# Performance work log

Measured on AMD Instinct MI355X. Metric: run time of the kernel, lower is better.

Reference implementation:

```python
import jax, jax.numpy as jnp
import numpy as np

N_NODES = 50000


def _gcn(x, row, col, w, b, n):
    # add self loops
    loops = jnp.arange(n, dtype=row.dtype)
    row = jnp.concatenate([row, loops])
    col = jnp.concatenate([col, loops])
    h = x @ w  # [N, out]
    deg = jax.ops.segment_sum(jnp.ones(col.shape, h.dtype), col, num_segments=n)
    dinv = jnp.where(deg > 0, deg ** -0.5, 0.0)
    norm = dinv[row] * dinv[col]  # [E+N]
    msg = norm[:, None] * h[row]
    out = jax.ops.segment_sum(msg, col, num_segments=n)
    return out + b


def _edgeconv(x, row, col, w1, b1, w2, b2, n):
    x_i = x[col]            # target features
    x_j = x[row]            # source features
    t = jnp.concatenate([x_i, x_j - x_i], axis=1)  # [E, 2*hidden]
    m = jax.nn.relu(t @ w1 + b1) @ w2 + b2          # [E, hidden]
    agg = jax.ops.segment_max(m, col, num_segments=n)
    # PyG fills empty segments with 0, segment_max fills with -inf
    return jnp.where(jnp.isfinite(agg), agg, 0.0)


def setup_inputs() -> dict:
    key = jax.random.key(0)
    ks = jax.random.split(key, 10)
    n, e = N_NODES, 800000
    cin, ch, cout = 32, 64, 16
    x = jax.random.normal(ks[0], (n, cin), dtype=jnp.float32)
    edge_index = jax.random.randint(ks[1], (2, e), 0, n, dtype=jnp.int64)

    def glorot(k, shape):
        lim = (6.0 / (shape[0] + shape[1])) ** 0.5
        return jax.random.uniform(k, shape, jnp.float32, -lim, lim)

    return {
        "x": x,
        "edge_index": edge_index,
        "gcn1_w": glorot(ks[2], (cin, ch)),
        "gcn1_b": jnp.zeros((ch,), jnp.float32),
        "edge_w1": glorot(ks[3], (2 * ch, ch)),
        "edge_b1": jnp.zeros((ch,), jnp.float32),
        "edge_w2": glorot(ks[4], (ch, ch)),
        "edge_b2": jnp.zeros((ch,), jnp.float32),
        "gcn2_w": glorot(ks[5], (ch, cout)),
        "gcn2_b": jnp.zeros((cout,), jnp.float32),
    }


def reference(x, edge_index, gcn1_w, gcn1_b, edge_w1, edge_b1, edge_w2, edge_b2, gcn2_w, gcn2_b):
    n = x.shape[0]
    row, col = edge_index[0], edge_index[1]
    h = jnp.tanh(_gcn(x, row, col, gcn1_w, gcn1_b, n))
    h = jax.nn.relu(_edgeconv(h, row, col, edge_w1, edge_b1, edge_w2, edge_b2, n))
    out = _gcn(h, row, col, gcn2_w, gcn2_b, n)
    return out
```

## Files before the change

### kernel.cpp

```cpp
#include <hip/hip_runtime.h>


typedef __attribute__((ext_vector_type(8))) short short8;
typedef __attribute__((ext_vector_type(4))) float f32x4;
typedef __attribute__((ext_vector_type(8))) _Float16 f16x8;
typedef __attribute__((ext_vector_type(4))) _Float16 f16x4;
typedef __attribute__((ext_vector_type(2))) _Float16 f16x2;

#define FILL_CH 4096

__device__ __forceinline__ unsigned short f2bf(float x) {
    unsigned int u = __float_as_uint(x);
    return (unsigned short)((u + 0x7FFFu + ((u >> 16) & 1u)) >> 16);
}
__device__ __forceinline__ float bf2f(unsigned short h) {
    return __uint_as_float(((unsigned int)h) << 16);
}
__device__ __forceinline__ void splitT(float u, short& hi, short& lo) {
    unsigned int ub = __float_as_uint(u);
    hi = (short)(ub >> 16);
    float r = u - __uint_as_float(ub & 0xFFFF0000u);
    lo = (short)(__float_as_uint(r) >> 16);
}
__device__ __forceinline__ f16x8 relu8(f16x8 v) {
    f16x8 z = {0, 0, 0, 0, 0, 0, 0, 0};
#if __has_builtin(__builtin_elementwise_max)
    return __builtin_elementwise_max(v, z);
#else
    f16x8 o;
#pragma unroll
    for (int j = 0; j < 8; ++j) o[j] = v[j] > (_Float16)0 ? v[j] : (_Float16)0;
    return o;
#endif
}

#define ROR_ADD(s, CTRL)                                                         \
    s += __int_as_float(__builtin_amdgcn_update_dpp(                             \
        0, __float_as_int(s), (CTRL), 0xf, 0xf, false))
#define ROR8_ADD(s) ROR_ADD(s, 0x128)

__global__ __launch_bounds__(256) void k_cast_count(
        const int* __restrict__ col, const float4* __restrict__ x4,
        f16x4* __restrict__ xh4, int* __restrict__ bcnt, int E, int m4, int nb) {
    __shared__ int cnt[512];
    int tid = threadIdx.x;
    for (int i = tid; i < nb; i += 256) cnt[i] = 0;
    __syncthreads();
    int e0 = blockIdx.x * FILL_CH;
#pragma unroll
    for (int i = 0; i < 16; ++i) {
        int e = e0 + tid + i * 256;
        if (e < E) atomicAdd(&cnt[col[e] >> 7], 1);
    }
    int nth = gridDim.x * 256;
    for (int idx = blockIdx.x * 256 + tid; idx < m4; idx += nth) {
        float4 v = x4[idx];
        f16x4 o;
        o[0] = (_Float16)v.x; o[1] = (_Float16)v.y;
        o[2] = (_Float16)v.z; o[3] = (_Float16)v.w;
        xh4[idx] = o;
    }
    __syncthreads();
    for (int i = tid; i < nb; i += 256)
        if (cnt[i]) atomicAdd(&bcnt[i], cnt[i]);
}

__global__ __launch_bounds__(512) void k_bucket_scan(
        const int* __restrict__ bcnt, int* __restrict__ bbase,
        int* __restrict__ bcur, int* __restrict__ ptr, int nb, int n, int E) {
    __shared__ int wt[8];
    int tid = threadIdx.x;
    int lane = tid & 63, w = tid >> 6;
    int v = (tid < nb) ? bcnt[tid] : 0;
    int s = v;
    for (int off = 1; off < 64; off <<= 1) {
        int t = __shfl_up(s, off, 64);
        if (lane >= off) s += t;
    }
    if (lane == 63) wt[w] = s;
    __syncthreads();
    int pre = 0;
    for (int i = 0; i < 8; ++i) if (i < w) pre += wt[i];
    int excl = pre + s - v;
    if (tid < nb) { bbase[tid] = excl; bcur[tid] = excl; }
    if (tid == nb) bbase[tid] = E;
    if (tid == 0) ptr[n] = E;
}

__global__ __launch_bounds__(256) void k_fill_a(const int* __restrict__ row,
                                                const int* __restrict__ col,
                                                int* __restrict__ bcur,
                                                int2* __restrict__ stage, int E, int nb) {
    __shared__ int cnt[512];
    __shared__ int base[512];
    int tid = threadIdx.x;
    int e0 = blockIdx.x * FILL_CH;
    for (int i = tid; i < nb; i += 256) cnt[i] = 0;
    __syncthreads();
    int r[16], c[16];
#pragma unroll
    for (int i = 0; i < 16; ++i) {
        int e = e0 + tid + i * 256;
        if (e < E) {
            r[i] = row[e]; c[i] = col[e];
            atomicAdd(&cnt[c[i] >> 7], 1);
        } else c[i] = -1;
    }
    __syncthreads();
    for (int i = tid; i < nb; i += 256)
        base[i] = cnt[i] ? atomicAdd(&bcur[i], cnt[i]) : 0;
    __syncthreads();
    for (int i = tid; i < nb; i += 256) cnt[i] = 0;
    __syncthreads();
#pragma unroll
    for (int i = 0; i < 16; ++i) {
        if (c[i] >= 0) {
            int b = c[i] >> 7;
            int lp = atomicAdd(&cnt[b], 1);
            stage[base[b] + lp] = make_int2(r[i], c[i]);
        }
    }
}

__global__ __launch_bounds__(256) void k_fill_b2(
        const int* __restrict__ bbase, const int* __restrict__ bcur_end,
        const int2* __restrict__ stage, int* __restrict__ ptr,
        float* __restrict__ dinv, int* __restrict__ csr, int n) {
    __shared__ int lcnt[128];
    __shared__ int lcur[128];
    __shared__ int wtotS;
    int b = blockIdx.x, tid = threadIdx.x;
    int c0 = b << 7;
    int start = bbase[b], end = bcur_end[b];
    if (tid < 128) lcnt[tid] = 0;
    __syncthreads();
    for (int p = start + tid; p < end; p += 256)
        atomicAdd(&lcnt[stage[p].y & 127], 1);
    __syncthreads();
    int lane = tid & 63, w = tid >> 6;
    int v = (tid < 128) ? lcnt[tid] : 0;
    int s = v;
    for (int off = 1; off < 64; off <<= 1) {
        int t = __shfl_up(s, off, 64);
        if (lane >= off) s += t;
    }
    if (tid == 63) wtotS = s;
    __syncthreads();
    int excl = s - v + ((w == 1) ? wtotS : 0);
    if (tid < 128) {
        int c = c0 + tid;
        int basep = start + excl;
        lcur[tid] = basep;
        if (c < n) {
            ptr[c] = basep;
            dinv[c] = rsqrtf((float)(v + 1));
        }
    }
    __syncthreads();
    for (int p = start + tid; p < end; p += 256) {
        int2 rc = stage[p];
        int pos = atomicAdd(&lcur[rc.y & 127], 1);
        csr[pos] = rc.x;
    }
}

__global__ __launch_bounds__(256) void k_gather32(
        const int* __restrict__ ptr, const int* __restrict__ csr_row,
        const float* __restrict__ x, const _Float16* __restrict__ xh,
        const float* __restrict__ dinv, float* __restrict__ agg, int n) {
    int wid = blockIdx.x * 4 + (threadIdx.x >> 6);
    if (wid >= n) return;
    int lane = threadIdx.x & 63;
    int f4 = lane & 7, slot = lane >> 3;
    int v = wid;
    int start = ptr[v], end = ptr[v + 1];
    const f16x4* xh4 = (const f16x4*)xh;
    float sx = 0.f, sy = 0.f, sz = 0.f, sw = 0.f;
    int p = start + slot;
    int r = (p < end) ? csr_row[p] : 0;
    while (p < end) {
        int rcur = r;
        int pn = p + 8;
        if (pn < end) r = csr_row[pn];
        float dr = dinv[rcur];
        f16x4 xv = xh4[(size_t)rcur * 8 + f4];
        sx = fmaf(dr, (float)xv[0], sx);
        sy = fmaf(dr, (float)xv[1], sy);
        sz = fmaf(dr, (float)xv[2], sz);
        sw = fmaf(dr, (float)xv[3], sw);
        p = pn;
    }
    ROR8_ADD(sx); ROR8_ADD(sy); ROR8_ADD(sz); ROR8_ADD(sw);
#pragma unroll
    for (int off = 16; off < 64; off <<= 1) {
        sx += __shfl_xor(sx, off); sy += __shfl_xor(sy, off);
        sz += __shfl_xor(sz, off); sw += __shfl_xor(sw, off);
    }
    if (slot == 0) {
        float dv = dinv[v], d2 = dv * dv;
        float4 xv = ((const float4*)x)[(size_t)v * 8 + f4];
        float4 o;
        o.x = dv * sx + d2 * xv.x;
        o.y = dv * sy + d2 * xv.y;
        o.z = dv * sz + d2 * xv.z;
        o.w = dv * sw + d2 * xv.w;
        ((float4*)agg)[(size_t)v * 8 + f4] = o;
    }
}

__global__ __launch_bounds__(256, 1) void k_h1tab(
        const float* __restrict__ agg, const float* __restrict__ gw,
        const float* __restrict__ gb, const float* __restrict__ w1,
        const float* __restrict__ b1,
        _Float16* __restrict__ atab, _Float16* __restrict__ btab, int ntiles) {
    __shared__ float tileS[4][16 * 66];
    int lane = threadIdx.x & 63;
    int wv = threadIdx.x >> 6;
    int n16 = lane & 15, q = lane >> 4;
    float* T = tileS[wv];

    short8 gh[4], gl[4];
    float gbias[4];
#pragma unroll
    for (int t = 0; t < 4; ++t) {
        gbias[t] = gb[t * 16 + n16];
        short8 hh, ll;
#pragma unroll
        for (int j = 0; j < 8; ++j) {
            float w = gw[(q * 8 + j) * 64 + t * 16 + n16];
            unsigned short wh = f2bf(w);
            hh[j] = (short)wh;
            ll[j] = (short)f2bf(w - bf2f(wh));
        }
        gh[t] = hh; gl[t] = ll;
    }
    short8 th[4][2], tl[4][2], uh[4][2], ul[4][2];
    float bias1[4];
#pragma unroll
    for (int t = 0; t < 4; ++t) {
        bias1[t] = b1[t * 16 + n16];
#pragma unroll
        for (int ck = 0; ck < 2; ++ck) {
            short8 h1v, l1v, h2v, l2v;
#pragma unroll
            for (int j = 0; j < 8; ++j) {
                int d = ck * 32 + q * 8 + j;
                float wbv = w1[(64 + d) * 64 + t * 16 + n16];
                float wtv = w1[d * 64 + t * 16 + n16] - wbv;
                unsigned short x1 = f2bf(wtv);
                h1v[j] = (short)x1; l1v[j] = (short)f2bf(wtv - bf2f(x1));
                unsigned short x2 = f2bf(wbv);
                h2v[j] = (short)x2; l2v[j] = (short)f2bf(wbv - bf2f(x2));
            }
            th[t][ck] = h1v; tl[t][ck] = l1v;
            uh[t][ck] = h2v; ul[t][ck] = l2v;
        }
    }

    int nwaves = gridDim.x * 4;
    int wid = blockIdx.x * 4 + wv;
    for (int tile = wid; tile < ntiles; tile += nwaves) {
        int v0 = tile * 16;
        const float4* a4 = (const float4*)(agg + (size_t)(v0 + n16) * 32);
        float4 A0 = a4[2 * q], A1 = a4[2 * q + 1];
        float a[8] = {A0.x, A0.y, A0.z, A0.w, A1.x, A1.y, A1.z, A1.w};
        short8 ah, al;
#pragma unroll
        for (int j = 0; j < 8; ++j) { short h, l; splitT(a[j], h, l); ah[j] = h; al[j] = l; }
#pragma unroll
        for (int t = 0; t < 4; ++t) {
            f32x4 acc = (f32x4){gbias[t], gbias[t], gbias[t], gbias[t]};
            acc = __builtin_amdgcn_mfma_f32_16x16x32_bf16(ah, gh[t], acc, 0, 0, 0);
            acc = __builtin_amdgcn_mfma_f32_16x16x32_bf16(al, gh[t], acc, 0, 0, 0);
            acc = __builtin_amdgcn_mfma_f32_16x16x32_bf16(ah, gl[t], acc, 0, 0, 0);
#pragma unroll
            for (int i = 0; i < 4; ++i)
                T[(q * 4 + i) * 66 + t * 16 + n16] = tanhf(acc[i]);
        }
        float b[16];
#pragma unroll
        for (int j = 0; j < 8; ++j) {
            b[j]     = T[n16 * 66 + q * 8 + j];
            b[8 + j] = T[n16 * 66 + 32 + q * 8 + j];
        }
        short8 ah0, ah1, al0, al1;
#pragma unroll
        for (int j = 0; j < 8; ++j) {
            short h, l;
            splitT(b[j], h, l);      ah0[j] = h; al0[j] = l;
            splitT(b[8 + j], h, l);  ah1[j] = h; al1[j] = l;
        }
#pragma unroll
        for (int t = 0; t < 4; ++t) {
            f32x4 aa = (f32x4){bias1[t], bias1[t], bias1[t], bias1[t]};
            aa = __builtin_amdgcn_mfma_f32_16x16x32_bf16(ah0, th[t][0], aa, 0, 0, 0);
            aa = __builtin_amdgcn_mfma_f32_16x16x32_bf16(ah1, th[t][1], aa, 0, 0, 0);
            aa = __builtin_amdgcn_mfma_f32_16x16x32_bf16(al0, th[t][0], aa, 0, 0, 0);
            aa = __builtin_amdgcn_mfma_f32_16x16x32_bf16(al1, th[t][1], aa, 0, 0, 0);
            aa = __builtin_amdgcn_mfma_f32_16x16x32_bf16(ah0, tl[t][0], aa, 0, 0, 0);
            aa = __builtin_amdgcn_mfma_f32_16x16x32_bf16(ah1, tl[t][1], aa, 0, 0, 0);
            f32x4 bb = (f32x4){0.f, 0.f, 0.f, 0.f};
            bb = __builtin_amdgcn_mfma_f32_16x16x32_bf16(ah0, uh[t][0], bb, 0, 0, 0);
            bb = __builtin_amdgcn_mfma_f32_16x16x32_bf16(ah1, uh[t][1], bb, 0, 0, 0);
            bb = __builtin_amdgcn_mfma_f32_16x16x32_bf16(al0, uh[t][0], bb, 0, 0, 0);
            bb = __builtin_amdgcn_mfma_f32_16x16x32_bf16(al1, uh[t][1], bb, 0, 0, 0);
            bb = __builtin_amdgcn_mfma_f32_16x16x32_bf16(ah0, ul[t][0], bb, 0, 0, 0);
            bb = __builtin_amdgcn_mfma_f32_16x16x32_bf16(ah1, ul[t][1], bb, 0, 0, 0);
#pragma unroll
            for (int i = 0; i < 4; ++i) {
                size_t off = (size_t)(v0 + q * 4 + i) * 64 + t * 16 + n16;
                atab[off] = (_Float16)aa[i];
                btab[off] = (_Float16)bb[i];
            }
        }
    }
}

__global__ __launch_bounds__(256) void k_edge_mlp(
        const int* __restrict__ ptr, const int* __restrict__ csr_row,
        const _Float16* __restrict__ atab, const _Float16* __restrict__ btab,
        const float* __restrict__ w2, const float* __restrict__ b2,
        const float* __restrict__ wg, _Float16* __restrict__ h2h, int n) {
    int lane = threadIdx.x & 63;
    int n16 = lane & 15, q = lane >> 4;

    f16x8 wh[4][2];
    float bias[4];
    float wgf[4][4];
#pragma unroll
    for (int t = 0; t < 4; ++t) {
        bias[t] = b2[t * 16 + n16];
#pragma unroll
        for (int jj = 0; jj < 4; ++jj)
            wgf[t][jj] = wg[(t * 16 + n16) * 16 + q * 4 + jj];
#pragma unroll
        for (int ck = 0; ck < 2; ++ck) {
            f16x8 hh;
#pragma unroll
            for (int j = 0; j < 8; ++j)
                hh[j] = (_Float16)w2[(ck * 32 + q * 8 + j) * 64 + t * 16 + n16];
            wh[t][ck] = hh;
        }
    }

    int nwaves = gridDim.x * 4;
    int wid = blockIdx.x * 4 + (threadIdx.x >> 6);

    for (int c = wid; c < n; c += nwaves) {
        int st = ptr[c], ed = ptr[c + 1];
        const f16x8* a8 = (const f16x8*)(atab + (size_t)c * 64);
        f16x8 A0 = a8[q], A1 = a8[4 + q];
        float red[4] = {0.f, 0.f, 0.f, 0.f};

        int p0 = st;
        int nfull = (ed - st) >> 4;
        for (int ft = 0; ft < nfull; ++ft, p0 += 16) {
            int r = csr_row[p0 + n16];
            const f16x8* b8 = (const f16x8*)(btab + (size_t)r * 64);
            f16x8 u0 = relu8(A0 + b8[q]);
            f16x8 u1 = relu8(A1 + b8[4 + q]);
#pragma unroll
            for (int t = 0; t < 4; ++t) {
                f32x4 acc = (f32x4){bias[t], bias[t], bias[t], bias[t]};
                acc = __builtin_amdgcn_mfma_f32_16x16x32_f16(u0, wh[t][0], acc, 0, 0, 0);
                acc = __builtin_amdgcn_mfma_f32_16x16x32_f16(u1, wh[t][1], acc, 0, 0, 0);
                red[t] = fmaxf(red[t], fmaxf(fmaxf(acc[0], acc[1]), fmaxf(acc[2], acc[3])));
            }
        }
        int rem = ed - p0;
        if (rem > 0) {
            f16x8 u0 = {0, 0, 0, 0, 0, 0, 0, 0};
            f16x8 u1 = {0, 0, 0, 0, 0, 0, 0, 0};
            if (n16 < rem) {
                int r = csr_row[p0 + n16];
                const f16x8* b8 = (const f16x8*)(btab + (size_t)r * 64);
                u0 = relu8(A0 + b8[q]);
                u1 = relu8(A1 + b8[4 + q]);
            }
#pragma unroll
            for (int t = 0; t < 4; ++t) {
                f32x4 acc = (f32x4){bias[t], bias[t], bias[t], bias[t]};
                acc = __builtin_amdgcn_mfma_f32_16x16x32_f16(u0, wh[t][0], acc, 0, 0, 0);
                acc = __builtin_amdgcn_mfma_f32_16x16x32_f16(u1, wh[t][1], acc, 0, 0, 0);
#pragma unroll
                for (int i = 0; i < 4; ++i)
                    if (q * 4 + i < rem) red[t] = fmaxf(red[t], acc[i]);
            }
        }
#pragma unroll
        for (int t = 0; t < 4; ++t) {
            red[t] = fmaxf(red[t], __shfl_xor(red[t], 16));
            red[t] = fmaxf(red[t], __shfl_xor(red[t], 32));
        }
        float part[4];
#pragma unroll
        for (int jj = 0; jj < 4; ++jj) {
            part[jj] = red[0] * wgf[0][jj];
            part[jj] = fmaf(red[1], wgf[1][jj], part[jj]);
            part[jj] = fmaf(red[2], wgf[2][jj], part[jj]);
            part[jj] = fmaf(red[3], wgf[3][jj], part[jj]);
            ROR_ADD(part[jj], 0x121);
            ROR_ADD(part[jj], 0x122);
            ROR_ADD(part[jj], 0x124);
            ROR_ADD(part[jj], 0x128);
        }
        if (n16 == 0) {
            f16x4 ph;
            ph[0] = (_Float16)part[0]; ph[1] = (_Float16)part[1];
            ph[2] = (_Float16)part[2]; ph[3] = (_Float16)part[3];
            ((f16x4*)(h2h + (size_t)c * 16))[q] = ph;
        }
    }
}

__global__ __launch_bounds__(256) void k_gcn2_gather(
        const int* __restrict__ ptr, const int* __restrict__ csr_row,
        const _Float16* __restrict__ h2h, const float* __restrict__ dinv,
        const float* __restrict__ bg, float* __restrict__ out, int n) {
    int wid = blockIdx.x * 4 + (threadIdx.x >> 6);
    if (wid >= n) return;
    int lane = threadIdx.x & 63;
    int f2 = lane & 7, slot = lane >> 3;
    int c = wid;
    int start = ptr[c], end = ptr[c + 1];
    const f16x2* h22 = (const f16x2*)h2h;
    float sx = 0.f, sy = 0.f;
    int p = start + slot;
    int r = (p < end) ? csr_row[p] : 0;
    while (p < end) {
        int rcur = r;
        int pn = p + 8;
        if (pn < end) r = csr_row[pn];
        float dr = dinv[rcur];
        f16x2 hv = h22[(size_t)rcur * 8 + f2];
        sx = fmaf(dr, (float)hv[0], sx);
        sy = fmaf(dr, (float)hv[1], sy);
        p = pn;
    }
    ROR8_ADD(sx); ROR8_ADD(sy);
#pragma unroll
    for (int off = 16; off < 64; off <<= 1) {
        sx += __shfl_xor(sx, off);
        sy += __shfl_xor(sy, off);
    }
    if (slot == 0) {
        float dv = dinv[c];
        f16x2 hv = h22[(size_t)c * 8 + f2];
        float2 o;
        o.x = bg[2 * f2]     + dv * (dv * (float)hv[0] + sx);
        o.y = bg[2 * f2 + 1] + dv * (dv * (float)hv[1] + sy);
        ((float2*)out)[(size_t)c * 8 + f2] = o;
    }
}

extern "C" void kernel_launch(void* const* d_in, const int* in_sizes, int n_in,
                              void* d_out, int out_size, void* d_ws, size_t ws_size,
                              hipStream_t stream) {
    const float* x   = (const float*)d_in[0];
    const int*   ei  = (const int*)d_in[1];
    const float* g1w = (const float*)d_in[2];
    const float* g1b = (const float*)d_in[3];
    const float* ew1 = (const float*)d_in[4];
    const float* eb1 = (const float*)d_in[5];
    const float* ew2 = (const float*)d_in[6];
    const float* eb2 = (const float*)d_in[7];
    const float* g2w = (const float*)d_in[8];
    const float* g2b = (const float*)d_in[9];
    float* out = (float*)d_out;
    float* ws  = (float*)d_ws;

    const int n = in_sizes[0] / 32;
    const int E = in_sizes[1] / 2;
    const int* row = ei;
    const int* col = ei + E;
    const int ntiles = (n + 15) / 16;
    const int nbuck = (n + 127) >> 7;

    size_t npad    = ((size_t)n + 63) & ~(size_t)63;
    size_t o_misc  = 0;
    size_t o_ptr   = npad;
    size_t o_csr   = o_ptr + npad + 64;
    size_t o_dinv  = o_csr + (size_t)E;
    size_t o_atab  = o_dinv + npad;
    size_t o_btab  = o_atab + (size_t)n * 32;
    size_t o_agg   = o_btab + (size_t)n * 32;
    size_t o_xh    = o_agg + (size_t)n * 32;
    size_t o_h2h   = o_xh + (size_t)n * 16;
    size_t o_stage = o_h2h + (size_t)n * 8;
    size_t o_bcur  = o_stage + (size_t)E * 2;

    int*      bcnt   = (int*)(ws + o_misc);
    int*      bbase  = (int*)(ws + o_misc) + 512;
    int*      ptr    = (int*)(ws + o_ptr);
    int*      csr    = (int*)(ws + o_csr);
    float*    dinv   = ws + o_dinv;
    _Float16* atab   = (_Float16*)(ws + o_atab);
    _Float16* btab   = (_Float16*)(ws + o_btab);
    float*    agg    = ws + o_agg;
    _Float16* xh     = (_Float16*)(ws + o_xh);
    _Float16* h2h    = (_Float16*)(ws + o_h2h);
    int2*     stage  = (int2*)(ws + o_stage);
    int*      bcur   = (int*)(ws + o_bcur);

    int nblk = (n + 3) / 4;
    int fill_nb = (E + FILL_CH - 1) / FILL_CH;
    int m4 = n * 8;

    hipMemsetAsync(bcnt, 0, 512 * sizeof(int), stream);
    k_cast_count<<<fill_nb, 256, 0, stream>>>(col, (const float4*)x, (f16x4*)xh,
                                              bcnt, E, m4, nbuck);
    k_bucket_scan<<<1, 512, 0, stream>>>(bcnt, bbase, bcur, ptr, nbuck, n, E);
    k_fill_a<<<fill_nb, 256, 0, stream>>>(row, col, bcur, stage, E, nbuck);
    k_fill_b2<<<nbuck, 256, 0, stream>>>(bbase, bcur, stage, ptr, dinv, csr, n);
    k_gather32<<<nblk, 256, 0, stream>>>(ptr, csr, x, xh, dinv, agg, n);
    k_h1tab<<<256, 256, 0, stream>>>(agg, g1w, g1b, ew1, eb1, atab, btab, ntiles);
    k_edge_mlp<<<2048, 256, 0, stream>>>(ptr, csr, atab, btab, ew2, eb2, g2w, h2h, n);
    k_gcn2_gather<<<nblk, 256, 0, stream>>>(ptr, csr, h2h, dinv, g2b, out, n);
}
```

Before: 200.9 us.

## Partition edge MLP by fixed edge chunks with shared-memory segment max

Replaces the node-per-wave edge MLP with a block-per-512-edges partition. Per-edge max results go into a shared-memory table using integer atomicMax, and nodes spanning chunk boundaries fall back to a global max buffer. A new binary-search kernel finds each chunk's node range and a fix-up kernel applies the final projection for boundary nodes. The goal is to fix load imbalance across high-degree and low-degree nodes and keep the MFMA tiles fully populated. The cost is an extra memset of a large n×64 buffer, global atomics, two extra kernel launches, and a per-edge target index array.

After: 227.8 us. +13.4%, slower.

```diff
diff --git a/kernel.cpp b/kernel.cpp
--- a/kernel.cpp
+++ b/kernel.cpp
@@ -8,6 +8,8 @@
 typedef __attribute__((ext_vector_type(2))) _Float16 f16x2;
 
 #define FILL_CH 4096
+#define TB_EDGES 512
+#define TBL 64
 
 __device__ __forceinline__ unsigned short f2bf(float x) {
     unsigned int u = __float_as_uint(x);
@@ -125,7 +127,8 @@
 __global__ __launch_bounds__(256) void k_fill_b2(
         const int* __restrict__ bbase, const int* __restrict__ bcur_end,
         const int2* __restrict__ stage, int* __restrict__ ptr,
-        float* __restrict__ dinv, int* __restrict__ csr, int n) {
+        float* __restrict__ dinv, int* __restrict__ csr,
+        int* __restrict__ cidx, int n) {
     __shared__ int lcnt[128];
     __shared__ int lcur[128];
     __shared__ int wtotS;
@@ -161,7 +164,22 @@
         int2 rc = stage[p];
         int pos = atomicAdd(&lcur[rc.y & 127], 1);
         csr[pos] = rc.x;
-    }
+        cidx[pos] = rc.y;
+    }
+}
+
+__global__ __launch_bounds__(256) void k_blo(const int* __restrict__ ptr,
+                                             int* __restrict__ blo, int n, int nblkE) {
+    int b = blockIdx.x * 256 + threadIdx.x;
+    if (b > nblkE) return;
+    if (b == nblkE) { blo[b] = n; return; }
+    int target = b * TB_EDGES;
+    int lo = 0, hi = n;
+    while (lo < hi) {
+        int mid = (lo + hi) >> 1;
+        if (ptr[mid] < target) lo = mid + 1; else hi = mid;
+    }
+    blo[b] = lo;
 }
 
 __global__ __launch_bounds__(256) void k_gather32(
@@ -317,22 +335,25 @@
 }
 
 __global__ __launch_bounds__(256) void k_edge_mlp(
-        const int* __restrict__ ptr, const int* __restrict__ csr_row,
+        const int* __restrict__ csr_row, const int* __restrict__ cidx,
+        const int* __restrict__ ptr, const int* __restrict__ blo,
         const _Float16* __restrict__ atab, const _Float16* __restrict__ btab,
         const float* __restrict__ w2, const float* __restrict__ b2,
-        const float* __restrict__ wg, _Float16* __restrict__ h2h, int n) {
-    int lane = threadIdx.x & 63;
+        const float* __restrict__ wg, int* __restrict__ gmax,
+        _Float16* __restrict__ h2h, int n, int E) {
+    __shared__ int tbl[TBL * 64];
+    int tid = threadIdx.x, lane = tid & 63, wv = tid >> 6;
     int n16 = lane & 15, q = lane >> 4;
+    int b = blockIdx.x;
+    int e0b = b * TB_EDGES;
+    int eend = min(e0b + TB_EDGES, E);
+    int cb = cidx[e0b];
 
     f16x8 wh[4][2];
     float bias[4];
-    float wgf[4][4];
 #pragma unroll
     for (int t = 0; t < 4; ++t) {
         bias[t] = b2[t * 16 + n16];
-#pragma unroll
-        for (int jj = 0; jj < 4; ++jj)
-            wgf[t][jj] = wg[(t * 16 + n16) * 16 + q * 4 + jj];
 #pragma unroll
         for (int ck = 0; ck < 2; ++ck) {
             f16x8 hh;
@@ -343,74 +364,168 @@
         }
     }
 
-    int nwaves = gridDim.x * 4;
-    int wid = blockIdx.x * 4 + (threadIdx.x >> 6);
-
-    for (int c = wid; c < n; c += nwaves) {
+    for (int i = tid; i < TBL * 64; i += 256) tbl[i] = 0;
+    __syncthreads();
+
+    int ntile = (eend - e0b + 15) >> 4;
+    int ti = wv;
+    if (ti < ntile) {
+        int ec = e0b + ti * 16 + n16;
+        if (ec >= eend) ec = eend - 1;
+        int r = csr_row[ec], cv = cidx[ec];
+        while (ti < ntile) {
+            int e0 = e0b + ti * 16;
+            int cvK = cv;
+            const f16x8* a8 = (const f16x8*)(atab + (size_t)cv * 64);
+            const f16x8* b8 = (const f16x8*)(btab + (size_t)r * 64);
+            f16x8 u0 = relu8(a8[q] + b8[q]);
+            f16x8 u1 = relu8(a8[4 + q] + b8[4 + q]);
+            int tin = ti + 4;
+            if (tin < ntile) {
+                int ec2 = e0b + tin * 16 + n16;
+                if (ec2 >= eend) ec2 = eend - 1;
+                r = csr_row[ec2]; cv = cidx[ec2];
+            }
+            f32x4 acc[4];
+#pragma unroll
+            for (int t = 0; t < 4; ++t) {
+                f32x4 a = (f32x4){bias[t], bias[t], bias[t], bias[t]};
+                a = __builtin_amdgcn_mfma_f32_16x16x32_f16(u0, wh[t][0], a, 0, 0, 0);
+                a = __builtin_amdgcn_mfma_f32_16x16x32_f16(u1, wh[t][1], a, 0, 0, 0);
+                acc[t] = a;
+            }
+            int c0l = __shfl(cvK, 0);
+            bool uni = __all(cvK == c0l) && (e0 + 15 < eend);
+            if (uni) {
+                float rr[4];
+#pragma unroll
+                for (int t = 0; t < 4; ++t) {
+                    float m = fmaxf(fmaxf(acc[t][0], acc[t][1]),
+                                    fmaxf(acc[t][2], acc[t][3]));
+                    m = fmaxf(m, __shfl_xor(m, 16));
+                    m = fmaxf(m, __shfl_xor(m, 32));
+                    rr[t] = fmaxf(m, 0.f);
+                }
+                if (q == 0) {
+                    int ix = c0l - cb;
+                    if ((unsigned)ix < (unsigned)TBL) {
+#pragma unroll
+                        for (int t = 0; t < 4; ++t)
+                            atomicMax(&tbl[ix * 64 + t * 16 + n16], __float_as_int(rr[t]));
+                    } else {
+#pragma unroll
+                        for (int t = 0; t < 4; ++t)
+                            atomicMax(&gmax[(size_t)c0l * 64 + t * 16 + n16],
+                                      __float_as_int(rr[t]));
+                    }
+                }
+            } else {
+                int cc0 = __shfl(cvK, q * 4 + 0);
+                int cc1 = __shfl(cvK, q * 4 + 1);
+                int cc2 = __shfl(cvK, q * 4 + 2);
+                int cc3 = __shfl(cvK, q * 4 + 3);
+                int e0q = e0 + q * 4;
+                float m[4];
+                int cur = cc0;
+                bool any = e0q < eend;
+#pragma unroll
+                for (int t = 0; t < 4; ++t) m[t] = fmaxf(acc[t][0], 0.f);
+                auto FLUSH = [&](int c) {
+                    int ix = c - cb;
+                    if ((unsigned)ix < (unsigned)TBL) {
+#pragma unroll
+                        for (int t = 0; t < 4; ++t)
+                            atomicMax(&tbl[ix * 64 + t * 16 + n16], __float_as_int(m[t]));
+                    } else {
+#pragma unroll
+                        for (int t = 0; t < 4; ++t)
+                            atomicMax(&gmax[(size_t)c * 64 + t * 16 + n16],
+                                      __float_as_int(m[t]));
+                    }
+                };
+                if (e0q + 1 < eend) {
+                    if (cc1 == cur) {
+#pragma unroll
+                        for (int t = 0; t < 4; ++t) m[t] = fmaxf(m[t], acc[t][1]);
+                    } else {
+                        FLUSH(cur); cur = cc1;
+#pragma unroll
+                        for (int t = 0; t < 4; ++t) m[t] = fmaxf(acc[t][1], 0.f);
+                    }
+                }
+                if (e0q + 2 < eend) {
+                    if (cc2 == cur) {
+#pragma unroll
+                        for (int t = 0; t < 4; ++t) m[t] = fmaxf(m[t], acc[t][2]);
+                    } else {
+                        FLUSH(cur); cur = cc2;
+#pragma unroll
+                        for (int t = 0; t < 4; ++t) m[t] = fmaxf(acc[t][2], 0.f);
+                    }
+                }
+                if (e0q + 3 < eend) {
+                    if (cc3 == cur) {
+#pragma unroll
+                        for (int t = 0; t < 4; ++t) m[t] = fmaxf(m[t], acc[t][3]);
+                    } else {
+                        FLUSH(cur); cur = cc3;
+#pragma unroll
+                        for (int t = 0; t < 4; ++t) m[t] = fmaxf(acc[t][3], 0.f);
+                    }
+                }
+                if (any) {
+#pragma unroll
+                    for (int t = 0; t < 4; ++t) m[t] = fmaxf(m[t], 0.f);
+                    FLUSH(cur);
+                }
+            }
+            ti = tin;
+        }
+    }
+    __syncthreads();
+
+    int clo = blo[b], chi = blo[b + 1];
+    int tmax = min(chi, cb + TBL);
+    for (int c = cb + wv * 4 + q; c < tmax; c += 16) {
+        int idx = c - cb;
         int st = ptr[c], ed = ptr[c + 1];
-        const f16x8* a8 = (const f16x8*)(atab + (size_t)c * 64);
-        f16x8 A0 = a8[q], A1 = a8[4 + q];
-        float red[4] = {0.f, 0.f, 0.f, 0.f};
-
-        int p0 = st;
-        int nfull = (ed - st) >> 4;
-        for (int ft = 0; ft < nfull; ++ft, p0 += 16) {
-            int r = csr_row[p0 + n16];
-            const f16x8* b8 = (const f16x8*)(btab + (size_t)r * 64);
-            f16x8 u0 = relu8(A0 + b8[q]);
-            f16x8 u1 = relu8(A1 + b8[4 + q]);
-#pragma unroll
-            for (int t = 0; t < 4; ++t) {
-                f32x4 acc = (f32x4){bias[t], bias[t], bias[t], bias[t]};
-                acc = __builtin_amdgcn_mfma_f32_16x16x32_f16(u0, wh[t][0], acc, 0, 0, 0);
-                acc = __builtin_amdgcn_mfma_f32_16x16x32_f16(u1, wh[t][1], acc, 0, 0, 0);
-                red[t] = fmaxf(red[t], fmaxf(fmaxf(acc[0], acc[1]), fmaxf(acc[2], acc[3])));
-            }
-        }
-        int rem = ed - p0;
-        if (rem > 0) {
-            f16x8 u0 = {0, 0, 0, 0, 0, 0, 0, 0};
-            f16x8 u1 = {0, 0, 0, 0, 0, 0, 0, 0};
-            if (n16 < rem) {
-                int r = csr_row[p0 + n16];
-                const f16x8* b8 = (const f16x8*)(btab + (size_t)r * 64);
-                u0 = relu8(A0 + b8[q]);
-                u1 = relu8(A1 + b8[4 + q]);
-            }
-#pragma unroll
-            for (int t = 0; t < 4; ++t) {
-                f32x4 acc = (f32x4){bias[t], bias[t], bias[t], bias[t]};
-                acc = __builtin_amdgcn_mfma_f32_16x16x32_f16(u0, wh[t][0], acc, 0, 0, 0);
-                acc = __builtin_amdgcn_mfma_f32_16x16x32_f16(u1, wh[t][1], acc, 0, 0, 0);
-#pragma unroll
-                for (int i = 0; i < 4; ++i)
-                    if (q * 4 + i < rem) red[t] = fmaxf(red[t], acc[i]);
-            }
-        }
-#pragma unroll
-        for (int t = 0; t < 4; ++t) {
-            red[t] = fmaxf(red[t], __shfl_xor(red[t], 16));
-            red[t] = fmaxf(red[t], __shfl_xor(red[t], 32));
-        }
-        float part[4];
-#pragma unroll
-        for (int jj = 0; jj < 4; ++jj) {
-            part[jj] = red[0] * wgf[0][jj];
-            part[jj] = fmaf(red[1], wgf[1][jj], part[jj]);
-            part[jj] = fmaf(red[2], wgf[2][jj], part[jj]);
-            part[jj] = fmaf(red[3], wgf[3][jj], part[jj]);
-            ROR_ADD(part[jj], 0x121);
-            ROR_ADD(part[jj], 0x122);
-            ROR_ADD(part[jj], 0x124);
-            ROR_ADD(part[jj], 0x128);
-        }
-        if (n16 == 0) {
-            f16x4 ph;
-            ph[0] = (_Float16)part[0]; ph[1] = (_Float16)part[1];
-            ph[2] = (_Float16)part[2]; ph[3] = (_Float16)part[3];
-            ((f16x4*)(h2h + (size_t)c * 16))[q] = ph;
-        }
-    }
+        bool bound = (c < clo) ||
+                     (ed > st && (st / TB_EDGES != (ed - 1) / TB_EDGES));
+        if (!bound) {
+            float s = 0.f;
+#pragma unroll
+            for (int d = 0; d < 64; ++d)
+                s = fmaf(__int_as_float(tbl[idx * 64 + d]), wg[d * 16 + n16], s);
+            h2h[(size_t)c * 16 + n16] = (_Float16)s;
+        } else {
+#pragma unroll
+            for (int t = 0; t < 4; ++t)
+                atomicMax(&gmax[(size_t)c * 64 + t * 16 + n16],
+                          tbl[idx * 64 + t * 16 + n16]);
+        }
+    }
+}
+
+__global__ __launch_bounds__(256) void k_bfix(
+        const int* __restrict__ ptr, const int* __restrict__ cidx,
+        const int* __restrict__ gmax, const float* __restrict__ wg,
+        _Float16* __restrict__ h2h, int n, int nblkE) {
+    int t = blockIdx.x * 256 + threadIdx.x;
+    int c = t >> 4, j = t & 15;
+    if (c >= n) return;
+    int st = ptr[c], ed = ptr[c + 1];
+    bool need = (ed > st) && (st / TB_EDGES != (ed - 1) / TB_EDGES);
+    if (!need) {
+        int owner = st / TB_EDGES;
+        if (owner >= nblkE) owner = nblkE - 1;
+        need = (c - cidx[owner * TB_EDGES]) >= TBL;
+    }
+    if (!need) return;
+    float s = 0.f;
+#pragma unroll
+    for (int d = 0; d < 64; ++d)
+        s = fmaf(__int_as_float(gmax[(size_t)c * 64 + d]), wg[d * 16 + j], s);
+    h2h[(size_t)c * 16 + j] = (_Float16)s;
 }
 
 __global__ __launch_bounds__(256) void k_gcn2_gather(
@@ -475,19 +590,22 @@
     const int* col = ei + E;
     const int ntiles = (n + 15) / 16;
     const int nbuck = (n + 127) >> 7;
+    const int nblkE = (E + TB_EDGES - 1) / TB_EDGES;
 
     size_t npad    = ((size_t)n + 63) & ~(size_t)63;
     size_t o_misc  = 0;
-    size_t o_ptr   = npad;
+    size_t o_ptr   = 1024;
     size_t o_csr   = o_ptr + npad + 64;
     size_t o_dinv  = o_csr + (size_t)E;
     size_t o_atab  = o_dinv + npad;
     size_t o_btab  = o_atab + (size_t)n * 32;
-    size_t o_agg   = o_btab + (size_t)n * 32;
+    size_t o_h2h   = o_btab + (size_t)n * 32;
+    size_t o_agg   = o_h2h + (size_t)n * 8;
     size_t o_xh    = o_agg + (size_t)n * 32;
-    size_t o_h2h   = o_xh + (size_t)n * 16;
-    size_t o_stage = o_h2h + (size_t)n * 8;
+    size_t o_stage = o_xh + (size_t)n * 16;
     size_t o_bcur  = o_stage + (size_t)E * 2;
+    size_t o_blo   = o_bcur + 512;
+    size_t o_cidx  = o_blo + 2048;
 
     int*      bcnt   = (int*)(ws + o_misc);
     int*      bbase  = (int*)(ws + o_misc) + 512;
@@ -496,11 +614,14 @@
     float*    dinv   = ws + o_dinv;
     _Float16* atab   = (_Float16*)(ws + o_atab);
     _Float16* btab   = (_Float16*)(ws + o_btab);
+    _Float16* h2h    = (_Float16*)(ws + o_h2h);
     float*    agg    = ws + o_agg;
+    int*      gmax   = (int*)(ws + o_agg);
     _Float16* xh     = (_Float16*)(ws + o_xh);
-    _Float16* h2h    = (_Float16*)(ws + o_h2h);
     int2*     stage  = (int2*)(ws + o_stage);
     int*      bcur   = (int*)(ws + o_bcur);
+    int*      blo    = (int*)(ws + o_blo);
+    int*      cidx   = (int*)(ws + o_cidx);
 
     int nblk = (n + 3) / 4;
     int fill_nb = (E + FILL_CH - 1) / FILL_CH;
@@ -511,9 +632,14 @@
                                               bcnt, E, m4, nbuck);
     k_bucket_scan<<<1, 512, 0, stream>>>(bcnt, bbase, bcur, ptr, nbuck, n, E);
     k_fill_a<<<fill_nb, 256, 0, stream>>>(row, col, bcur, stage, E, nbuck);
-    k_fill_b2<<<nbuck, 256, 0, stream>>>(bbase, bcur, stage, ptr, dinv, csr, n);
+    k_fill_b2<<<nbuck, 256, 0, stream>>>(bbase, bcur, stage, ptr, dinv, csr, cidx, n);
+    k_blo<<<(nblkE + 256) / 256, 256, 0, stream>>>(ptr, blo, n, nblkE);
     k_gather32<<<nblk, 256, 0, stream>>>(ptr, csr, x, xh, dinv, agg, n);
     k_h1tab<<<256, 256, 0, stream>>>(agg, g1w, g1b, ew1, eb1, atab, btab, ntiles);
-    k_edge_mlp<<<2048, 256, 0, stream>>>(ptr, csr, atab, btab, ew2, eb2, g2w, h2h, n);
+    hipMemsetAsync(gmax, 0, (size_t)n * 64 * sizeof(int), stream);
+    k_edge_mlp<<<nblkE, 256, 0, stream>>>(csr, cidx, ptr, blo, atab, btab,
+                                          ew2, eb2, g2w, gmax, h2h, n, E);
+    k_bfix<<<(n * 16 + 255) / 256, 256, 0, stream>>>(ptr, cidx, gmax, g2w, h2h,
+                                                     n, nblkE);
     k_gcn2_gather<<<nblk, 256, 0, stream>>>(ptr, csr, h2h, dinv, g2b, out, n);
 }
```
